# Optimization experiments

Hardware: AMD Instinct MI355X
Metric: run time of the kernel (lower is better)

Reference implementation:

```python
import jax, jax.numpy as jnp
import numpy as np

N, IN_DIM, OUT_DIM, NUM_HOPS, SD = 8192, 256, 256, 4, 64
ETA, LAM_LAP, LAM_SP, EPS = 0.5, 0.3, 0.05, 0.5
LN_EPS = 1e-5


def setup_inputs() -> dict:
    key = jax.random.key(0)
    ks = jax.random.split(key, 6)
    K = NUM_HOPS + 1
    return {
        "H": jax.random.normal(ks[0], (N, IN_DIM), jnp.float32),
        "hops": jax.random.normal(ks[1], (K, N, IN_DIM), jnp.float32),
        "L": jax.random.normal(ks[2], (N, N), jnp.float32),
        "U": jax.random.normal(ks[3], (K, IN_DIM, SD), jnp.float32) * 0.1,
        "W_in": jax.random.normal(ks[4], (OUT_DIM, IN_DIM), jnp.float32) * 0.05,
        "ln_gamma": jnp.ones((OUT_DIM,), jnp.float32),
        "ln_beta": jnp.zeros((OUT_DIM,), jnp.float32),
        "log_tau": jnp.zeros((), jnp.float32),
    }


def _per_hop(U_k, H_k):
    n = H_k.shape[0]
    Q, _ = jnp.linalg.qr(U_k)                 # [in_dim, sd]
    Z = Q.T @ H_k.T                           # [sd, n]
    G = Z @ Z.T                               # [sd, sd] Gram, reused
    Sigma = G / (n + 1e-8)
    tr_S = jnp.trace(Sigma)
    tr_S2 = jnp.sum(Sigma * Sigma)            # trace(Sigma @ Sigma), Sigma symmetric
    rank_eff = tr_S ** 2 / (tr_S2 + 1e-8)
    coeff = SD / (n * EPS ** 2 + 1e-8)
    M = jnp.eye(SD, dtype=Z.dtype) + coeff * G
    Lc = jnp.linalg.cholesky(M)
    MiZ = jax.scipy.linalg.cho_solve((Lc, True), Z)  # [sd, n]
    grad_R = (Q @ MiZ).T                      # [n, in_dim]
    return rank_eff, grad_R


def reference(H, hops, L, U, W_in, ln_gamma, ln_beta, log_tau):
    tau = jnp.clip(jnp.exp(log_tau), 0.1, 10.0)
    rank_effs, grads_R = jax.vmap(_per_hop)(U, hops)      # [K], [K,n,in_dim]
    lap_terms = jnp.einsum('nm,kmd->knd', L, hops)        # [K,n,in_dim]
    w = jax.nn.softmax(rank_effs / tau)                   # [K]
    grad_sum = jnp.einsum('k,knd->nd', w, grads_R)
    lap_sum = jnp.einsum('k,knd->nd', w, lap_terms)
    H_half = H + ETA * grad_sum - ETA * LAM_LAP * lap_sum
    H_prox = jnp.sign(H_half) * jax.nn.relu(jnp.abs(H_half) - LAM_SP * ETA)
    H_out = H_prox @ W_in.T
    mu = jnp.mean(H_out, axis=-1, keepdims=True)
    var = jnp.var(H_out, axis=-1, keepdims=True)
    H_out = (H_out - mu) * jax.lax.rsqrt(var + LN_EPS) * ln_gamma + ln_beta
    return H_out, rank_effs, w
```

## Files before the change

### kernel.cpp

```cpp
#include <hip/hip_runtime.h>
#include <stdint.h>


typedef __attribute__((ext_vector_type(8))) short  s16x8;
typedef __attribute__((ext_vector_type(4))) float  f32x4;

#define NNODE 8192
#define DIN   256
#define KHOP  5
#define SDM   64

static const size_t OFF_Q    = 0;
static const size_t OFF_QT   = OFF_Q   + (size_t)5*256*64*4;
static const size_t OFF_ZT   = OFF_QT  + (size_t)5*64*256*2;
static const size_t OFF_GP   = OFF_ZT  + (size_t)5*8192*64*2;
static const size_t OFF_LM   = OFF_GP  + (size_t)5*16*4096*4;
static const size_t OFF_RD   = OFF_LM  + (size_t)5*4096*4;
static const size_t OFF_LU   = OFF_RD  + (size_t)5*64*4;
static const size_t OFF_RDU  = OFF_LU  + (size_t)5*4096*4;
static const size_t OFF_RE   = OFF_RDU + (size_t)5*64*4;
static const size_t OFF_W    = OFF_RE  + 64;
static const size_t OFF_T2   = OFF_W   + 64;
static const size_t OFF_HWT  = OFF_T2  + (size_t)5*256*64*2;
static const size_t OFF_WBF  = OFF_HWT + (size_t)256*8192*2;
static const size_t OFF_HP   = OFF_WBF + (size_t)256*256*2;
static const size_t OFF_PART = OFF_HP  + (size_t)8192*256*2;

__device__ __forceinline__ unsigned short f2bf(float f){
  unsigned u = __builtin_bit_cast(unsigned, f);
  u += 0x7FFFu + ((u >> 16) & 1u);
  return (unsigned short)(u >> 16);
}
__device__ __forceinline__ float bf2f(unsigned h){
  return __builtin_bit_cast(float, h << 16);
}
__device__ __forceinline__ void gl_lds16(const void* g, void* l){
  __builtin_amdgcn_global_load_lds(
      (const __attribute__((address_space(1))) void*)g,
      (__attribute__((address_space(3))) void*)l, 16, 0, 0);
}
__device__ __forceinline__ f32x4 mfma16(s16x8 a, s16x8 b, f32x4 c){
  return __builtin_amdgcn_mfma_f32_16x16x32_bf16(a, b, c, 0, 0, 0);
}

__device__ __forceinline__ void wave_chol64(float* a, float& rdk, int lane){
  rdk = 0.0f;
  #pragma unroll
  for (int j = 0; j < 64; ++j){
    float dj  = __shfl(a[j], j);
    float d   = sqrtf(fmaxf(dj, 1e-20f));
    float rdj = 1.0f / d;
    float cj  = a[j] * rdj;
    a[j] = cj;
    if (lane == j) rdk = rdj;
    #pragma unroll
    for (int l = j+1; l < 64; ++l)
      a[l] -= cj * __shfl(cj, l);
  }
}

__global__ __launch_bounds__(256) void k_pre(const float* __restrict__ U,
                                             float* __restrict__ Lu,
                                             float* __restrict__ rdu){
  __shared__ float A[64*65];
  int tid = threadIdx.x;
  int k = blockIdx.x;
  const float* Uk = U + (size_t)k*16384;
  int ti = tid >> 4, tj = tid & 15;
  float s[16];
  #pragma unroll
  for (int i = 0; i < 16; ++i) s[i] = 0.0f;
  for (int n = 0; n < 256; ++n){
    f32x4 xa = *(const f32x4*)(Uk + n*64 + ti*4);
    f32x4 xb = *(const f32x4*)(Uk + n*64 + tj*4);
    #pragma unroll
    for (int p = 0; p < 4; ++p)
      #pragma unroll
      for (int q = 0; q < 4; ++q) s[p*4+q] += xa[p]*xb[q];
  }
  #pragma unroll
  for (int p = 0; p < 4; ++p)
    #pragma unroll
    for (int q = 0; q < 4; ++q) A[(ti*4+p)*65 + tj*4+q] = s[p*4+q];
  __syncthreads();
  if (tid < 64){
    int lane = tid;
    float a[64];
    #pragma unroll
    for (int l = 0; l < 64; ++l) a[l] = A[lane*65 + l];
    float rdk;
    wave_chol64(a, rdk, lane);
    #pragma unroll
    for (int l = 0; l < 64; ++l) Lu[(size_t)k*4096 + lane*64 + l] = a[l];
    rdu[k*64 + lane] = rdk;
  }
}

__global__ __launch_bounds__(256) void k_qsolve(const float* __restrict__ U,
                                                const float* __restrict__ Lu,
                                                const float* __restrict__ rdu,
                                                float* __restrict__ Qf,
                                                unsigned short* __restrict__ Qt){
  int k = blockIdx.y, tid = threadIdx.x, wave = tid >> 6, lane = tid & 63;
  __shared__ float Al[64*65];
  __shared__ float rds[64];
  for (int e = tid; e < 4096; e += 256) Al[(e>>6)*65 + (e&63)] = Lu[(size_t)k*4096 + e];
  if (tid < 64) rds[tid] = rdu[k*64 + tid];
  __syncthreads();
  int n = blockIdx.x*4 + wave;
  float x = U[((size_t)k*256 + n)*64 + lane];
  #pragma unroll
  for (int j = 0; j < 64; ++j){
    float zj = __shfl(x, j) * rds[j];
    x = (lane == j) ? zj : (lane > j ? x - Al[lane*65+j]*zj : x);
  }
  Qf[((size_t)k*256 + n)*64 + lane] = x;
  Qt[(size_t)k*16384 + lane*256 + n] = f2bf(x);
}

__global__ __launch_bounds__(256,2) void k_zgemm(const float* __restrict__ hops,
                                                 const unsigned short* __restrict__ Qt,
                                                 unsigned short* __restrict__ Zt){
  __shared__ __align__(16) unsigned short Al[128][72];
  __shared__ __align__(16) unsigned short Bl[64][64];
  int tid = threadIdx.x, lane = tid & 63, wave = tid >> 6;
  int q = lane >> 4, r = lane & 15;
  int k = blockIdx.y, m0 = blockIdx.x * 128;
  f32x4 acc[2][4];
  #pragma unroll
  for (int a = 0; a < 2; ++a)
    #pragma unroll
    for (int b = 0; b < 4; ++b) acc[a][b] = (f32x4){0,0,0,0};
  int rr = tid >> 1, half = tid & 1;
  for (int it = 0; it < 4; ++it){
    __syncthreads();
    #pragma unroll
    for (int i = 0; i < 2; ++i){
      int o = i*4096 + wave*1024 + lane*16;
      int srow = o >> 7, kc = (o & 127) >> 1;
      gl_lds16(Qt + (size_t)k*16384 + srow*256 + it*64 + kc,
               (char*)&Bl[0][0] + i*4096 + wave*1024);
    }
    const float* ga = hops + ((size_t)k*NNODE + m0 + rr)*256 + it*64 + half*32;
    f32x4 v[8];
    #pragma unroll
    for (int i = 0; i < 8; ++i) v[i] = *(const f32x4*)(ga + i*4);
    #pragma unroll
    for (int i = 0; i < 4; ++i){
      s16x8 t;
      #pragma unroll
      for (int j = 0; j < 8; ++j){ int e = i*8+j; t[j] = (short)f2bf(v[e>>2][e&3]); }
      *(s16x8*)&Al[rr][half*32 + i*8] = t;
    }
    __syncthreads();
    #pragma unroll
    for (int h = 0; h < 2; ++h){
      int ko = h*32 + q*8;
      s16x8 b[4];
      #pragma unroll
      for (int ni = 0; ni < 4; ++ni) b[ni] = *(const s16x8*)&Bl[ni*16 + r][ko];
      #pragma unroll
      for (int mi = 0; mi < 2; ++mi){
        s16x8 a = *(const s16x8*)&Al[wave*32 + mi*16 + r][ko];
        #pragma unroll
        for (int ni = 0; ni < 4; ++ni) acc[mi][ni] = mfma16(a, b[ni], acc[mi][ni]);
      }
    }
  }
  #pragma unroll
  for (int mi = 0; mi < 2; ++mi)
    #pragma unroll
    for (int ni = 0; ni < 4; ++ni)
      #pragma unroll
      for (int ii = 0; ii < 4; ++ii){
        int m = m0 + wave*32 + mi*16 + q*4 + ii;
        int sc = ni*16 + r;
        Zt[((size_t)k*NNODE + m)*64 + sc] = f2bf(acc[mi][ni][ii]);
      }
}

__global__ __launch_bounds__(256) void k_gpart(const unsigned short* __restrict__ Zt,
                                               float* __restrict__ Gp){
  int k = blockIdx.x, c = blockIdx.y, tid = threadIdx.x;
  __shared__ __align__(16) unsigned short Zl[128][64];
  int ti = tid >> 4, tj = tid & 15;
  float acc[16];
  #pragma unroll
  for (int i = 0; i < 16; ++i) acc[i] = 0.0f;
  for (int sub = 0; sub < 4; ++sub){
    const char* gb = (const char*)Zt + ((size_t)k*NNODE + c*512 + sub*128)*128;
    __syncthreads();
    #pragma unroll
    for (int i = 0; i < 4; ++i){
      int o = i*4096 + tid*16;
      *(uint4*)((char*)&Zl[0][0] + o) = *(const uint4*)(gb + o);
    }
    __syncthreads();
    for (int n = 0; n < 128; ++n){
      const unsigned short* row = &Zl[n][0];
      uint2 ua = *(const uint2*)(row + ti*4);
      uint2 ub = *(const uint2*)(row + tj*4);
      float xa[4] = { bf2f(ua.x & 0xffff), bf2f(ua.x >> 16), bf2f(ua.y & 0xffff), bf2f(ua.y >> 16) };
      float xb[4] = { bf2f(ub.x & 0xffff), bf2f(ub.x >> 16), bf2f(ub.y & 0xffff), bf2f(ub.y >> 16) };
      #pragma unroll
      for (int p = 0; p < 4; ++p)
        #pragma unroll
        for (int qn = 0; qn < 4; ++qn) acc[p*4+qn] += xa[p]*xb[qn];
    }
  }
  float* o = Gp + ((size_t)k*16 + c)*4096;
  #pragma unroll
  for (int p = 0; p < 4; ++p)
    #pragma unroll
    for (int qn = 0; qn < 4; ++qn) o[(ti*4+p)*64 + tj*4+qn] = acc[p*4+qn];
}

__global__ __launch_bounds__(256) void k_gred(const float* __restrict__ Gp,
                                              float* __restrict__ LmO,
                                              float* __restrict__ rdO,
                                              float* __restrict__ reO){
  int k = blockIdx.x, tid = threadIdx.x;
  __shared__ float A[64*65];
  __shared__ float red[256];
  int ti = tid >> 4, tj = tid & 15;
  float s[16];
  #pragma unroll
  for (int i = 0; i < 16; ++i) s[i] = 0.0f;
  for (int c = 0; c < 16; ++c){
    const float* g = Gp + ((size_t)k*16 + c)*4096 + (ti*4)*64 + tj*4;
    #pragma unroll
    for (int p = 0; p < 4; ++p)
      #pragma unroll
      for (int qn = 0; qn < 4; ++qn) s[p*4+qn] += g[p*64+qn];
  }
  const float sc    = 1.0f / (8192.0f + 1e-8f);
  const float coeff = 64.0f / (8192.0f*0.25f + 1e-8f);
  float trp = 0.0f, tr2p = 0.0f;
  #pragma unroll
  for (int p = 0; p < 4; ++p)
    #pragma unroll
    for (int qn = 0; qn < 4; ++qn){
      float gg = s[p*4+qn];
      float sg = gg * sc;
      tr2p += sg*sg;
      int row = ti*4+p, col = tj*4+qn;
      if (row == col) trp += sg;
      A[row*65 + col] = (row == col ? 1.0f : 0.0f) + coeff*gg;
    }
  red[tid] = trp; __syncthreads();
  for (int o = 128; o > 0; o >>= 1){ if (tid < o) red[tid] += red[tid+o]; __syncthreads(); }
  float tr = red[0]; __syncthreads();
  red[tid] = tr2p; __syncthreads();
  for (int o = 128; o > 0; o >>= 1){ if (tid < o) red[tid] += red[tid+o]; __syncthreads(); }
  float tr2 = red[0];
  if (tid == 0) reO[k] = tr*tr / (tr2 + 1e-8f);
  __syncthreads();
  if (tid < 64){
    int lane = tid;
    float a[64];
    #pragma unroll
    for (int l = 0; l < 64; ++l) a[l] = A[lane*65 + l];
    float rdk;
    wave_chol64(a, rdk, lane);
    #pragma unroll
    for (int l = 0; l < 64; ++l) LmO[(size_t)k*4096 + lane*64 + l] = a[l];
    rdO[k*64 + lane] = rdk;
  }
}

__global__ void k_soft(const float* __restrict__ re, const float* __restrict__ ltau,
                       float* __restrict__ wv, float* __restrict__ dtail){
  if (threadIdx.x == 0){
    float tau = expf(ltau[0]);
    tau = fminf(fmaxf(tau, 0.1f), 10.0f);
    float r[5], m = -1e30f;
    for (int i = 0; i < 5; ++i){ r[i] = re[i]; m = fmaxf(m, r[i]); }
    float e[5], sum = 0.0f;
    for (int i = 0; i < 5; ++i){ e[i] = expf((r[i]-m)/tau); sum += e[i]; }
    for (int i = 0; i < 5; ++i){
      float w = e[i]/sum;
      wv[i] = w; dtail[i] = r[i]; dtail[5+i] = w;
    }
  }
}

__global__ __launch_bounds__(256) void k_post(const float* __restrict__ hops,
                                              const float* __restrict__ wv,
                                              unsigned short* __restrict__ hwT,
                                              const float* __restrict__ Qf,
                                              const float* __restrict__ LmI,
                                              const float* __restrict__ rdI,
                                              unsigned short* __restrict__ T2w,
                                              const float* __restrict__ Win,
                                              unsigned short* __restrict__ Wbf){
  __shared__ float T[64*65];
  __shared__ float rds[64];
  int bid = blockIdx.x, tid = threadIdx.x;
  if (bid < 512){
    int n0 = (bid & 127)*64, d0 = (bid >> 7)*64;
    float wl[5];
    #pragma unroll
    for (int k = 0; k < 5; ++k) wl[k] = -0.15f * wv[k];
    for (int e = tid; e < 1024; e += 256){
      int row = e >> 4, c4 = (e & 15)*4;
      f32x4 acc = (f32x4){0,0,0,0};
      #pragma unroll
      for (int k = 0; k < 5; ++k){
        f32x4 v = *(const f32x4*)(hops + ((size_t)k*NNODE + n0 + row)*256 + d0 + c4);
        acc += v * wl[k];
      }
      T[row*65 + c4+0] = acc[0]; T[row*65 + c4+1] = acc[1];
      T[row*65 + c4+2] = acc[2]; T[row*65 + c4+3] = acc[3];
    }
    __syncthreads();
    for (int e = tid; e < 1024; e += 256){
      int dr = e >> 4, c4 = (e & 15)*4;
      unsigned short h0 = f2bf(T[(c4+0)*65 + dr]);
      unsigned short h1 = f2bf(T[(c4+1)*65 + dr]);
      unsigned short h2 = f2bf(T[(c4+2)*65 + dr]);
      unsigned short h3 = f2bf(T[(c4+3)*65 + dr]);
      uint2 u; u.x = (unsigned)h0 | ((unsigned)h1 << 16); u.y = (unsigned)h2 | ((unsigned)h3 << 16);
      *(uint2*)(hwT + (size_t)(d0+dr)*NNODE + n0 + c4) = u;
    }
  } else if (bid < 832){
    int i = bid - 512;
    int k = i >> 6, xb = i & 63;
    int wave = tid >> 6, lane = tid & 63;
    for (int e = tid; e < 4096; e += 256) T[(e>>6)*65 + (e&63)] = LmI[(size_t)k*4096 + e];
    if (tid < 64) rds[tid] = rdI[k*64 + tid];
    __syncthreads();
    int n = xb*4 + wave;
    float x = Qf[((size_t)k*256 + n)*64 + lane];
    #pragma unroll
    for (int j = 0; j < 64; ++j){
      float zj = __shfl(x, j) * rds[j];
      x = (lane == j) ? zj : (lane > j ? x - T[lane*65+j]*zj : x);
    }
    #pragma unroll
    for (int j = 63; j >= 0; --j){
      float yj = __shfl(x, j) * rds[j];
      x = (lane == j) ? yj : (lane < j ? x - T[j*65+lane]*yj : x);
    }
    float scale = 0.5f * wv[k];
    T2w[((size_t)k*256 + n)*64 + lane] = f2bf(scale * x);
  } else {
    int i = bid - 832;
    int e = (i*256 + tid)*4;
    f32x4 v = *(const f32x4*)(Win + e);
    uint2 u;
    u.x = (unsigned)f2bf(v[0]) | ((unsigned)f2bf(v[1]) << 16);
    u.y = (unsigned)f2bf(v[2]) | ((unsigned)f2bf(v[3]) << 16);
    *(uint2*)(Wbf + e) = u;
  }
}

__global__ __launch_bounds__(256,2) void k_gg(const float* __restrict__ Lf,
                                              const unsigned short* __restrict__ Bt,
                                              unsigned short* __restrict__ part,
                                              const unsigned short* __restrict__ Zt,
                                              const unsigned short* __restrict__ T2w){
  __shared__ __align__(16) unsigned short SM[24960];
  int bid = blockIdx.x, tid = threadIdx.x;
  int lane = tid & 63, wave = tid >> 6;
  int q = lane >> 4, r = lane & 15;
  if (bid < 512){
    unsigned short* Al = SM;
    unsigned short* Bl = SM + 16*520;
    int m0 = (bid & 63) * 128;
    int by = bid >> 6;
    size_t kbase = (size_t)by * 1024;
    int sr = lane >> 3, sc8 = (lane & 7) * 8;
    int ar = tid >> 1, ah = tid & 1;
    unsigned short* adst = Al + (ar>>3)*520 + (ar&7)*64 + ah*32;
    const float* abase = Lf + (size_t)(m0 + ar)*NNODE + ah*32;
    f32x4 acc[8][4];
    #pragma unroll
    for (int a = 0; a < 8; ++a)
      #pragma unroll
      for (int b = 0; b < 4; ++b) acc[a][b] = (f32x4){0,0,0,0};
    f32x4 av[8];
    #pragma unroll
    for (int j = 0; j < 8; ++j) av[j] = *(const f32x4*)(abase + kbase + j*4);
    #pragma unroll
    for (int i = 0; i < 8; ++i){
      int cb = i*4 + wave;
      gl_lds16(Bt + (size_t)(cb*8 + sr)*NNODE + kbase + sc8,
               (char*)Bl + cb*1040 + lane*16);
    }
    #pragma unroll
    for (int j = 0; j < 4; ++j){
      s16x8 t;
      #pragma unroll
      for (int e = 0; e < 8; ++e) t[e] = (short)f2bf(av[j*2 + (e>>2)][e&3]);
      *(s16x8*)(adst + j*8) = t;
    }
    __syncthreads();
    for (int it = 0; it < 16; ++it){
      size_t k1 = kbase + (it+1)*64;
      if (it < 15){
        #pragma unroll
        for (int j = 0; j < 8; ++j) av[j] = *(const f32x4*)(abase + k1 + j*4);
      }
      #pragma unroll
      for (int h = 0; h < 2; ++h){
        int ko = h*32 + q*8;
        s16x8 b[4];
        #pragma unroll
        for (int ni = 0; ni < 4; ++ni){
          int d = wave*64 + ni*16 + r;
          b[ni] = *(const s16x8*)(Bl + (d>>3)*520 + (d&7)*64 + ko);
        }
        #pragma unroll
        for (int mi = 0; mi < 8; ++mi){
          int m = mi*16 + r;
          s16x8 a = *(const s16x8*)(Al + (m>>3)*520 + (m&7)*64 + ko);
          #pragma unroll
          for (int ni = 0; ni < 4; ++ni) acc[mi][ni] = mfma16(a, b[ni], acc[mi][ni]);
        }
      }
      __syncthreads();
      if (it < 15){
        #pragma unroll
        for (int i = 0; i < 8; ++i){
          int cb = i*4 + wave;
          gl_lds16(Bt + (size_t)(cb*8 + sr)*NNODE + k1 + sc8,
                   (char*)Bl + cb*1040 + lane*16);
        }
        #pragma unroll
        for (int j = 0; j < 4; ++j){
          s16x8 t;
          #pragma unroll
          for (int e = 0; e < 8; ++e) t[e] = (short)f2bf(av[j*2 + (e>>2)][e&3]);
          *(s16x8*)(adst + j*8) = t;
        }
      }
      __syncthreads();
    }
    unsigned short* o = part + (size_t)by * 2097152;
    #pragma unroll
    for (int mi = 0; mi < 8; ++mi)
      #pragma unroll
      for (int ni = 0; ni < 4; ++ni)
        #pragma unroll
        for (int ii = 0; ii < 4; ++ii){
          int m = m0 + mi*16 + q*4 + ii;
          int n = wave*64 + ni*16 + r;
          o[(size_t)m*256 + n] = f2bf(acc[mi][ni][ii]);
        }
  } else {
    unsigned short* Al = SM;
    unsigned short* Bl = SM + 2048;
    int m0 = (bid - 512) * 32;
    f32x4 acc[2][4];
    #pragma unroll
    for (int a = 0; a < 2; ++a)
      #pragma unroll
      for (int b = 0; b < 4; ++b) acc[a][b] = (f32x4){0,0,0,0};
    for (int kk = 0; kk < 5; ++kk){
      __syncthreads();
      {
        int o = wave*1024 + lane*16;
        gl_lds16((const char*)Zt + ((size_t)kk*NNODE + m0)*128 + o,
                 (char*)Al + wave*1024);
      }
      #pragma unroll
      for (int i = 0; i < 8; ++i){
        int o = i*4096 + wave*1024 + lane*16;
        gl_lds16((const char*)T2w + (size_t)kk*32768 + o,
                 (char*)Bl + i*4096 + wave*1024);
      }
      __syncthreads();
      #pragma unroll
      for (int h = 0; h < 2; ++h){
        int ko = h*32 + q*8;
        s16x8 b[4];
        #pragma unroll
        for (int ni = 0; ni < 4; ++ni) b[ni] = *(const s16x8*)&Bl[(wave*64 + ni*16 + r)*64 + ko];
        #pragma unroll
        for (int mi = 0; mi < 2; ++mi){
          s16x8 a = *(const s16x8*)&Al[(mi*16 + r)*64 + ko];
          #pragma unroll
          for (int ni = 0; ni < 4; ++ni) acc[mi][ni] = mfma16(a, b[ni], acc[mi][ni]);
        }
      }
    }
    unsigned short* o8 = part + (size_t)8 * 2097152;
    #pragma unroll
    for (int mi = 0; mi < 2; ++mi)
      #pragma unroll
      for (int ni = 0; ni < 4; ++ni)
        #pragma unroll
        for (int ii = 0; ii < 4; ++ii){
          int m = m0 + mi*16 + q*4 + ii;
          int n = wave*64 + ni*16 + r;
          o8[(size_t)m*256 + n] = f2bf(acc[mi][ni][ii]);
        }
  }
}

__global__ __launch_bounds__(256,2) void k_finln(const float* __restrict__ H,
                                                 const unsigned short* __restrict__ part,
                                                 const unsigned short* __restrict__ Wbf,
                                                 const float* __restrict__ gamma,
                                                 const float* __restrict__ beta,
                                                 float* __restrict__ out){
  __shared__ __align__(16) unsigned short Hl[64][264];
  __shared__ __align__(16) unsigned short Bl[256][64];
  __shared__ float SmR[64][4];
  __shared__ float SqR[64][4];
  int tid = threadIdx.x, lane = tid & 63, wave = tid >> 6;
  int q = lane >> 4, r = lane & 15;
  int m0 = blockIdx.x * 64;
  #define PROX(a) ({ float _t = fabsf(a) - 0.025f; _t > 0.0f ? copysignf(_t,(a)) : 0.0f; })
  for (int g = tid; g < 4096; g += 256){
    int row = g >> 6, c4 = (g & 63) * 4;
    size_t e = (size_t)(m0 + row)*256 + c4;
    f32x4 h = *(const f32x4*)(H + e);
    float s0 = h[0], s1 = h[1], s2 = h[2], s3 = h[3];
    #pragma unroll
    for (int sl = 0; sl < 9; ++sl){
      uint2 u = *(const uint2*)(part + (size_t)sl*2097152 + e);
      s0 += bf2f(u.x & 0xffff); s1 += bf2f(u.x >> 16);
      s2 += bf2f(u.y & 0xffff); s3 += bf2f(u.y >> 16);
    }
    uint2 o;
    o.x = (unsigned)f2bf(PROX(s0)) | ((unsigned)f2bf(PROX(s1)) << 16);
    o.y = (unsigned)f2bf(PROX(s2)) | ((unsigned)f2bf(PROX(s3)) << 16);
    *(uint2*)&Hl[row][c4] = o;
  }
  f32x4 acc[4][4];
  #pragma unroll
  for (int a = 0; a < 4; ++a)
    #pragma unroll
    for (int b = 0; b < 4; ++b) acc[a][b] = (f32x4){0,0,0,0};
  for (int it = 0; it < 4; ++it){
    __syncthreads();
    #pragma unroll
    for (int i = 0; i < 8; ++i){
      int o = i*4096 + wave*1024 + lane*16;
      int n = o >> 7, kc = o & 127;
      gl_lds16((const char*)Wbf + (size_t)n*512 + it*128 + kc,
               (char*)&Bl[0][0] + i*4096 + wave*1024);
    }
    __syncthreads();
    #pragma unroll
    for (int h = 0; h < 2; ++h){
      int ko = it*64 + h*32 + q*8;
      s16x8 b[4];
      #pragma unroll
      for (int ni = 0; ni < 4; ++ni) b[ni] = *(const s16x8*)&Bl[wave*64 + ni*16 + r][h*32 + q*8];
      #pragma unroll
      for (int mi = 0; mi < 4; ++mi){
        s16x8 a = *(const s16x8*)&Hl[mi*16 + r][ko];
        #pragma unroll
        for (int ni = 0; ni < 4; ++ni) acc[mi][ni] = mfma16(a, b[ni], acc[mi][ni]);
      }
    }
  }
  #pragma unroll
  for (int mi = 0; mi < 4; ++mi)
    #pragma unroll
    for (int ii = 0; ii < 4; ++ii){
      float sm = 0.0f, sq = 0.0f;
      #pragma unroll
      for (int ni = 0; ni < 4; ++ni){
        float v = acc[mi][ni][ii];
        sm += v; sq += v*v;
      }
      #pragma unroll
      for (int o = 1; o < 16; o <<= 1){ sm += __shfl_xor(sm, o, 64); sq += __shfl_xor(sq, o, 64); }
      if (r == 0){
        int rl = mi*16 + q*4 + ii;
        SmR[rl][wave] = sm; SqR[rl][wave] = sq;
      }
    }
  __syncthreads();
  float g[4], b[4];
  #pragma unroll
  for (int ni = 0; ni < 4; ++ni){
    g[ni] = gamma[wave*64 + ni*16 + r];
    b[ni] = beta [wave*64 + ni*16 + r];
  }
  #pragma unroll
  for (int mi = 0; mi < 4; ++mi)
    #pragma unroll
    for (int ii = 0; ii < 4; ++ii){
      int rl = mi*16 + q*4 + ii;
      float sm = SmR[rl][0] + SmR[rl][1] + SmR[rl][2] + SmR[rl][3];
      float sq = SqR[rl][0] + SqR[rl][1] + SqR[rl][2] + SqR[rl][3];
      float mean = sm * (1.0f/256.0f);
      float var  = sq * (1.0f/256.0f) - mean*mean;
      float rs   = rsqrtf(var + 1e-5f);
      #pragma unroll
      for (int ni = 0; ni < 4; ++ni){
        out[(size_t)(m0+rl)*256 + wave*64 + ni*16 + r] =
            (acc[mi][ni][ii] - mean)*rs*g[ni] + b[ni];
      }
    }
}

extern "C" void kernel_launch(void* const* d_in, const int* in_sizes, int n_in,
                              void* d_out, int out_size, void* d_ws, size_t ws_size,
                              hipStream_t stream){
  const float* H    = (const float*)d_in[0];
  const float* hops = (const float*)d_in[1];
  const float* Lmat = (const float*)d_in[2];
  const float* U    = (const float*)d_in[3];
  const float* Win  = (const float*)d_in[4];
  const float* gam  = (const float*)d_in[5];
  const float* bet  = (const float*)d_in[6];
  const float* ltau = (const float*)d_in[7];
  float* out = (float*)d_out;

  char* ws = (char*)d_ws;
  float*          Qf   = (float*)(ws + OFF_Q);
  unsigned short* Qt   = (unsigned short*)(ws + OFF_QT);
  unsigned short* Zt   = (unsigned short*)(ws + OFF_ZT);
  float*          Gp   = (float*)(ws + OFF_GP);
  float*          Lm   = (float*)(ws + OFF_LM);
  float*          rdw  = (float*)(ws + OFF_RD);
  float*          Lu   = (float*)(ws + OFF_LU);
  float*          rdu  = (float*)(ws + OFF_RDU);
  float*          re   = (float*)(ws + OFF_RE);
  float*          wv   = (float*)(ws + OFF_W);
  unsigned short* T2w  = (unsigned short*)(ws + OFF_T2);
  unsigned short* hwT  = (unsigned short*)(ws + OFF_HWT);
  unsigned short* Wbf  = (unsigned short*)(ws + OFF_WBF);
  unsigned short* part = (unsigned short*)(ws + OFF_PART);

  hipLaunchKernelGGL(k_pre,    dim3(5),      dim3(256), 0, stream, U, Lu, rdu);
  hipLaunchKernelGGL(k_qsolve, dim3(64,5),   dim3(256), 0, stream, U, Lu, rdu, Qf, Qt);
  hipLaunchKernelGGL(k_zgemm,  dim3(64,5),   dim3(256), 0, stream, hops, Qt, Zt);
  hipLaunchKernelGGL(k_gpart,  dim3(5,16),   dim3(256), 0, stream, Zt, Gp);
  hipLaunchKernelGGL(k_gred,   dim3(5),      dim3(256), 0, stream, Gp, Lm, rdw, re);
  hipLaunchKernelGGL(k_soft,   dim3(1),      dim3(64),  0, stream, re, ltau, wv, out + 2097152);
  hipLaunchKernelGGL(k_post,   dim3(896),    dim3(256), 0, stream, hops, wv, hwT, Qf, Lm, rdw, T2w, Win, Wbf);
  hipLaunchKernelGGL(k_gg,     dim3(768),    dim3(256), 0, stream, Lmat, hwT, part, Zt, T2w);
  hipLaunchKernelGGL(k_finln,  dim3(128),    dim3(256), 0, stream, H, part, Wbf, gam, bet, out);
}
```

Measured before the change: 657.0 us.

## Double-buffer L and B tiles in LDS for the Laplacian GEMM

Converts the Laplacian GEMM main loop in k_gg from a single LDS buffer with two barriers per iteration to ping-pong A/B buffers with one barrier. The next tile's global loads and async B copies are issued before the MFMA work on the current tile, and the fp32-to-bf16 conversion is written to the other buffer afterwards. The A-tile load mapping also changes to match the B row/column pattern. This doubles LDS use, so launch bounds drop from 2 to 1 blocks per SM, which trades occupancy for overlap.

Result: no change. 662.2 us (+0.8%).

```diff
diff --git a/kernel.cpp b/kernel.cpp
--- a/kernel.cpp
+++ b/kernel.cpp
@@ -354,52 +354,75 @@
   }
 }
 
-__global__ __launch_bounds__(256,2) void k_gg(const float* __restrict__ Lf,
+__global__ __launch_bounds__(256,1) void k_gg(const float* __restrict__ Lf,
                                               const unsigned short* __restrict__ Bt,
                                               unsigned short* __restrict__ part,
                                               const unsigned short* __restrict__ Zt,
                                               const unsigned short* __restrict__ T2w){
-  __shared__ __align__(16) unsigned short SM[24960];
+  __shared__ __align__(16) unsigned short SM[49920];
   int bid = blockIdx.x, tid = threadIdx.x;
   int lane = tid & 63, wave = tid >> 6;
   int q = lane >> 4, r = lane & 15;
   if (bid < 512){
-    unsigned short* Al = SM;
-    unsigned short* Bl = SM + 16*520;
+    unsigned short* A0 = SM;
+    unsigned short* B0 = SM + 16*520;
+    unsigned short* A1 = SM + 48*520;
+    unsigned short* B1 = SM + 64*520;
     int m0 = (bid & 63) * 128;
     int by = bid >> 6;
     size_t kbase = (size_t)by * 1024;
     int sr = lane >> 3, sc8 = (lane & 7) * 8;
-    int ar = tid >> 1, ah = tid & 1;
-    unsigned short* adst = Al + (ar>>3)*520 + (ar&7)*64 + ah*32;
-    const float* abase = Lf + (size_t)(m0 + ar)*NNODE + ah*32;
     f32x4 acc[8][4];
     #pragma unroll
     for (int a = 0; a < 8; ++a)
       #pragma unroll
       for (int b = 0; b < 4; ++b) acc[a][b] = (f32x4){0,0,0,0};
-    f32x4 av[8];
-    #pragma unroll
-    for (int j = 0; j < 8; ++j) av[j] = *(const f32x4*)(abase + kbase + j*4);
-    #pragma unroll
-    for (int i = 0; i < 8; ++i){
-      int cb = i*4 + wave;
-      gl_lds16(Bt + (size_t)(cb*8 + sr)*NNODE + kbase + sc8,
-               (char*)Bl + cb*1040 + lane*16);
-    }
-    #pragma unroll
-    for (int j = 0; j < 4; ++j){
-      s16x8 t;
-      #pragma unroll
-      for (int e = 0; e < 8; ++e) t[e] = (short)f2bf(av[j*2 + (e>>2)][e&3]);
-      *(s16x8*)(adst + j*8) = t;
-    }
-    __syncthreads();
-    for (int it = 0; it < 16; ++it){
-      size_t k1 = kbase + (it+1)*64;
-      if (it < 15){
-        #pragma unroll
-        for (int j = 0; j < 8; ++j) av[j] = *(const f32x4*)(abase + k1 + j*4);
+    {
+      f32x4 av[4][2];
+      #pragma unroll
+      for (int i = 0; i < 4; ++i){
+        int c = i*4 + wave;
+        const float* p = Lf + (size_t)(m0 + c*8 + sr)*NNODE + kbase + sc8;
+        av[i][0] = *(const f32x4*)p;
+        av[i][1] = *(const f32x4*)(p + 4);
+      }
+      #pragma unroll
+      for (int i = 0; i < 8; ++i){
+        int cb = i*4 + wave;
+        gl_lds16(Bt + (size_t)(cb*8 + sr)*NNODE + kbase + sc8,
+                 (char*)B0 + cb*1040 + lane*16);
+      }
+      #pragma unroll
+      for (int i = 0; i < 4; ++i){
+        int c = i*4 + wave;
+        s16x8 t;
+        #pragma unroll
+        for (int e = 0; e < 8; ++e) t[e] = (short)f2bf(av[i][e>>2][e&3]);
+        *(s16x8*)((char*)A0 + c*1040 + lane*16) = t;
+      }
+      __syncthreads();
+    }
+    for (int t = 0; t < 16; ++t){
+      unsigned short* Ac = (t & 1) ? A1 : A0;
+      unsigned short* Bc = (t & 1) ? B1 : B0;
+      unsigned short* An = (t & 1) ? A0 : A1;
+      unsigned short* Bn = (t & 1) ? B0 : B1;
+      size_t kn = kbase + (size_t)(t+1)*64;
+      f32x4 av[4][2];
+      if (t < 15){
+        #pragma unroll
+        for (int i = 0; i < 4; ++i){
+          int c = i*4 + wave;
+          const float* p = Lf + (size_t)(m0 + c*8 + sr)*NNODE + kn + sc8;
+          av[i][0] = *(const f32x4*)p;
+          av[i][1] = *(const f32x4*)(p + 4);
+        }
+        #pragma unroll
+        for (int i = 0; i < 8; ++i){
+          int cb = i*4 + wave;
+          gl_lds16(Bt + (size_t)(cb*8 + sr)*NNODE + kn + sc8,
+                   (char*)Bn + cb*1040 + lane*16);
+        }
       }
       #pragma unroll
       for (int h = 0; h < 2; ++h){
@@ -408,30 +431,24 @@
         #pragma unroll
         for (int ni = 0; ni < 4; ++ni){
           int d = wave*64 + ni*16 + r;
-          b[ni] = *(const s16x8*)(Bl + (d>>3)*520 + (d&7)*64 + ko);
+          b[ni] = *(const s16x8*)(Bc + (d>>3)*520 + (d&7)*64 + ko);
         }
         #pragma unroll
         for (int mi = 0; mi < 8; ++mi){
           int m = mi*16 + r;
-          s16x8 a = *(const s16x8*)(Al + (m>>3)*520 + (m&7)*64 + ko);
+          s16x8 a = *(const s16x8*)(Ac + (m>>3)*520 + (m&7)*64 + ko);
           #pragma unroll
           for (int ni = 0; ni < 4; ++ni) acc[mi][ni] = mfma16(a, b[ni], acc[mi][ni]);
         }
       }
-      __syncthreads();
-      if (it < 15){
-        #pragma unroll
-        for (int i = 0; i < 8; ++i){
-          int cb = i*4 + wave;
-          gl_lds16(Bt + (size_t)(cb*8 + sr)*NNODE + k1 + sc8,
-                   (char*)Bl + cb*1040 + lane*16);
-        }
-        #pragma unroll
-        for (int j = 0; j < 4; ++j){
-          s16x8 t;
+      if (t < 15){
+        #pragma unroll
+        for (int i = 0; i < 4; ++i){
+          int c = i*4 + wave;
+          s16x8 tt;
           #pragma unroll
-          for (int e = 0; e < 8; ++e) t[e] = (short)f2bf(av[j*2 + (e>>2)][e&3]);
-          *(s16x8*)(adst + j*8) = t;
+          for (int e = 0; e < 8; ++e) tt[e] = (short)f2bf(av[i][e>>2][e&3]);
+          *(s16x8*)((char*)An + c*1040 + lane*16) = tt;
         }
       }
       __syncthreads();
```
